# Optimization experiments

Measured on AMD Instinct MI355X. Metric: run time of the kernel, lower is better.

The kernel has to match this reference:

```python
import jax, jax.numpy as jnp
import numpy as np
import math

N = 50000      # nodes
E = 800000     # edges
D = 128        # hidden_dim
H = 8          # num_heads
HD = D // H    # head_dim
EPS = 1e-5


def setup_inputs() -> dict:
    key = jax.random.key(0)
    ks = jax.random.split(key, 24)
    s = 0.02
    inp = {
        "x": jax.random.normal(ks[0], (N, D), jnp.float32),
        "edge_index": jax.random.randint(ks[1], (2, E), 0, N, jnp.int64),
        "edge_attr": jax.random.normal(ks[2], (E, D), jnp.float32),
        # attention projections (stored [in, out]; torch Linear is x @ W.T + b)
        "Wq": jax.random.normal(ks[3], (D, D), jnp.float32) * s,
        "bq": jnp.zeros((D,), jnp.float32),
        "Wk": jax.random.normal(ks[4], (D, D), jnp.float32) * s,
        "bk": jnp.zeros((D,), jnp.float32),
        "Wv": jax.random.normal(ks[5], (D, D), jnp.float32) * s,
        "bv": jnp.zeros((D,), jnp.float32),
        "Wo": jax.random.normal(ks[6], (D, D), jnp.float32) * s,
        "bo": jnp.zeros((D,), jnp.float32),
        # edge-feature -> per-head score bias
        "We": jax.random.normal(ks[7], (D, H), jnp.float32) * s,
        "be": jnp.zeros((H,), jnp.float32),
        # FFN
        "W1": jax.random.normal(ks[8], (D, 4 * D), jnp.float32) * s,
        "bf1": jnp.zeros((4 * D,), jnp.float32),
        "W2": jax.random.normal(ks[9], (4 * D, D), jnp.float32) * s,
        "bf2": jnp.zeros((D,), jnp.float32),
        # layer norms
        "g1": jnp.ones((D,), jnp.float32),
        "beta1": jnp.zeros((D,), jnp.float32),
        "g2": jnp.ones((D,), jnp.float32),
        "beta2": jnp.zeros((D,), jnp.float32),
    }
    return inp


def _layer_norm(x, g, b):
    m = jnp.mean(x, axis=-1, keepdims=True)
    v = jnp.mean(jnp.square(x - m), axis=-1, keepdims=True)
    return (x - m) * jax.lax.rsqrt(v + EPS) * g + b


def reference(x, edge_index, edge_attr, Wq, bq, Wk, bk, Wv, bv, Wo, bo,
              We, be, W1, bf1, W2, bf2, g1, beta1, g2, beta2):
    row, col = edge_index[0], edge_index[1]

    # --- pre-norm attention block ---
    xn = _layer_norm(x, g1, beta1)
    Q = (xn @ Wq + bq).reshape(N, H, HD)
    K = (xn @ Wk + bk).reshape(N, H, HD)
    V = (xn @ Wv + bv).reshape(N, H, HD)

    # per-edge dot-product scores [E, H]
    scores = jnp.einsum('ehd,ehd->eh', Q[row], K[col]) / math.sqrt(HD)
    scores = scores + edge_attr @ We + be

    # segment softmax over edges grouped by destination node `row`
    smax = jax.ops.segment_max(scores, row, num_segments=N)  # [N, H]
    smax = jax.lax.stop_gradient(smax)
    ex = jnp.exp(scores - smax[row])
    denom = jax.ops.segment_sum(ex, row, num_segments=N)     # [N, H]
    alpha = ex / denom[row]                                  # [E, H]

    # weighted scatter-add aggregation [N, H, HD]
    agg = jax.ops.segment_sum(V[col] * alpha[..., None], row, num_segments=N)
    attn_out = agg.reshape(N, D) @ Wo + bo
    x = x + attn_out

    # --- pre-norm FFN block ---
    xn2 = _layer_norm(x, g2, beta2)
    h = jax.nn.gelu(xn2 @ W1 + bf1, approximate=False)
    x = x + (h @ W2 + bf2)
    return x
```

## Files before the change

kernel.cpp:

```cpp
#include <hip/hip_runtime.h>
#include <hip/hip_bf16.h>
#include <math.h>

#define NNODES 50000
#define NEDGES 800000
#define DIM 128
#define NH 8

#define NEG_SENTINEL -3.0e38f

typedef __attribute__((ext_vector_type(8))) short bf16x8_t;
typedef __attribute__((ext_vector_type(4))) float f32x4_t;

__device__ __forceinline__ float gelu_exact(float v) {
    return 0.5f * v * (1.0f + erff(v * 0.70710678118654752f));
}
__device__ __forceinline__ ushort bfbits(float f) {
    uint u = __float_as_uint(f);
    u += 0x7fffu + ((u >> 16) & 1u);
    return (ushort)(u >> 16);
}
__device__ __forceinline__ uint pack2(float a, float b) {
    return (uint)bfbits(a) | ((uint)bfbits(b) << 16);
}
__device__ __forceinline__ float lo16(uint u) { return __uint_as_float(u << 16); }
__device__ __forceinline__ float hi16(uint u) { return __uint_as_float(u & 0xffff0000u); }
__device__ __forceinline__ float b2f(ushort u) { return __uint_as_float(((uint)u) << 16); }

__global__ void zero_counts(int* __restrict__ counts) {
    int i = blockIdx.x * 256 + threadIdx.x;
    if (i < NNODES) counts[i] = 0;
}

__global__ void setup_kernel(const int* __restrict__ ei, int* __restrict__ counts,
                             int* __restrict__ rank,
                             const float* __restrict__ Wq, const float* __restrict__ Wk,
                             const float* __restrict__ Wv, const float* __restrict__ Wo,
                             const float* __restrict__ W1, const float* __restrict__ W2,
                             const float* __restrict__ We,
                             const float* __restrict__ bq, const float* __restrict__ bk,
                             const float* __restrict__ bv,
                             ushort* __restrict__ wt4, ushort* __restrict__ w1t,
                             ushort* __restrict__ w2t, ushort* __restrict__ wet,
                             float* __restrict__ b384) {
    int b = blockIdx.x;
    if (b < NEDGES / 256) {
        int e = b * 256 + threadIdx.x;
        rank[e] = atomicAdd(&counts[ei[e]], 1);
        return;
    }
    int i = (b - NEDGES / 256) * 256 + threadIdx.x;
    if (i < 65536) {
        int w = i >> 14, j = i & 16383;
        int c = j >> 7, k = j & 127;
        const float* src = (w == 0) ? Wq : (w == 1) ? Wk : (w == 2) ? Wv : Wo;
        wt4[i] = bfbits(src[k * 128 + c]);
    } else if (i < 131072) {
        int j = i - 65536;
        int c = j >> 7, k = j & 127;
        w1t[j] = bfbits(W1[k * 512 + c]);
    } else if (i < 196608) {
        int j = i - 131072;
        int c = j >> 9, k = j & 511;
        w2t[j] = bfbits(W2[k * 128 + c]);
    } else if (i < 198656) {
        int j = i - 196608;
        int h = j >> 7, k = j & 127;
        wet[j] = (h < 8) ? bfbits(We[k * 8 + h]) : (ushort)0;
    } else if (i < 198656 + 384) {
        int j = i - 198656;
        b384[j] = (j < 128) ? bq[j] : (j < 256) ? bk[j - 128] : bv[j - 256];
    }
}

__global__ __launch_bounds__(256)
void ln_qkv_kernel(const float* __restrict__ x, const float* __restrict__ g1,
                   const float* __restrict__ b1, const ushort* __restrict__ wt4,
                   const float* __restrict__ b384, ushort* __restrict__ Qb,
                   uint* __restrict__ KVp, int M) {
    __shared__ ushort An[64 * 128];
    __shared__ ushort Ws[64 * 128];
    int tid = threadIdx.x, lane = tid & 63, wave = tid >> 6;
    int row0b = blockIdx.x * 64;
    int sr = lane >> 4;
    int sl = lane & 15;
    char* WsB = reinterpret_cast<char*>(Ws);
    float4 ga = reinterpret_cast<const float4*>(g1)[sl * 2];
    float4 gb = reinterpret_cast<const float4*>(g1)[sl * 2 + 1];
    float4 ba = reinterpret_cast<const float4*>(b1)[sl * 2];
    float4 bbv = reinterpret_cast<const float4*>(b1)[sl * 2 + 1];
    #pragma unroll
    for (int g = 0; g < 4; ++g) {
        int rl = wave * 16 + g * 4 + sr;
        int srow = min(row0b + rl, M - 1);
        const float4* xp = reinterpret_cast<const float4*>(x + (size_t)srow * 128 + sl * 8);
        float4 a = xp[0], b = xp[1];
        float s  = ((a.x + a.y) + (a.z + a.w)) + ((b.x + b.y) + (b.z + b.w));
        float sq = ((a.x*a.x + a.y*a.y) + (a.z*a.z + a.w*a.w)) +
                   ((b.x*b.x + b.y*b.y) + (b.z*b.z + b.w*b.w));
        #pragma unroll
        for (int mm = 1; mm < 16; mm <<= 1) {
            s  += __shfl_xor(s, mm, 64);
            sq += __shfl_xor(sq, mm, 64);
        }
        float mean = s * (1.0f / DIM);
        float var  = sq * (1.0f / DIM) - mean * mean;
        float rs = rsqrtf(var + 1e-5f);
        uint4 pk;
        pk.x = pack2((a.x - mean) * rs * ga.x + ba.x, (a.y - mean) * rs * ga.y + ba.y);
        pk.y = pack2((a.z - mean) * rs * ga.z + ba.z, (a.w - mean) * rs * ga.w + ba.w);
        pk.z = pack2((b.x - mean) * rs * gb.x + bbv.x, (b.y - mean) * rs * gb.y + bbv.y);
        pk.w = pack2((b.z - mean) * rs * gb.z + bbv.z, (b.w - mean) * rs * gb.w + bbv.w);
        int byte = rl * 256 + ((sl * 16) ^ ((rl & 7) << 4));
        *reinterpret_cast<uint4*>(reinterpret_cast<char*>(An) + byte) = pk;
    }
    __builtin_amdgcn_wave_barrier();
    int er = lane & 15, kg = lane >> 4;
    int lrow = wave * 16 + er;
    int rsw = (er & 7) << 4;
    bf16x8_t afN[4];
    #pragma unroll
    for (int ks = 0; ks < 4; ++ks)
        afN[ks] = *reinterpret_cast<const bf16x8_t*>(
            reinterpret_cast<char*>(An) + lrow * 256 + ((ks * 64 + kg * 16) ^ rsw));
    f32x4_t acc[24];
    #pragma unroll
    for (int f = 0; f < 24; ++f) acc[f] = (f32x4_t){0.f, 0.f, 0.f, 0.f};
    #pragma unroll
    for (int st = 0; st < 6; ++st) {
        __syncthreads();
        #pragma unroll
        for (int it = 0; it < 4; ++it) {
            int idx = it * 256 + tid;
            int col = idx >> 4, ch = idx & 15;
            uint4 d = *reinterpret_cast<const uint4*>(wt4 + (size_t)(st * 64 + col) * 128 + ch * 8);
            *reinterpret_cast<uint4*>(WsB + col * 256 + ((ch * 16) ^ ((col & 7) << 4))) = d;
        }
        __syncthreads();
        #pragma unroll
        for (int ks = 0; ks < 4; ++ks) {
            #pragma unroll
            for (int fl = 0; fl < 4; ++fl) {
                int fc = fl * 16 + er;
                bf16x8_t bfr = *reinterpret_cast<const bf16x8_t*>(
                    WsB + fc * 256 + ((ks * 64 + kg * 16) ^ ((fc & 7) << 4)));
                acc[st * 4 + fl] = __builtin_amdgcn_mfma_f32_16x16x32_bf16(afN[ks], bfr, acc[st * 4 + fl], 0, 0, 0);
            }
        }
    }
    #pragma unroll
    for (int f = 0; f < 24; ++f) {
        int col = (f >> 2) * 64 + (f & 3) * 16 + er;
        float bc = b384[col];
        #pragma unroll
        for (int r = 0; r < 4; ++r) {
            int row = row0b + wave * 16 + kg * 4 + r;
            if (row < M) {
                float v = acc[f][r] + bc;
                if (col < 128) {
                    Qb[(size_t)row * 128 + col] = bfbits(v);
                } else if (col < 256) {
                    reinterpret_cast<ushort*>(KVp + (size_t)row * 128 + (col - 128))[0] = bfbits(v);
                } else {
                    reinterpret_cast<ushort*>(KVp + (size_t)row * 128 + (col - 256))[1] = bfbits(v);
                }
            }
        }
    }
}

__global__ __launch_bounds__(256)
void wo_ffn_kernel(const ushort* __restrict__ A, const ushort* __restrict__ woT,
                   const float* __restrict__ bo, const float* __restrict__ xres,
                   const float* __restrict__ g2, const float* __restrict__ b2,
                   const ushort* __restrict__ w1t, const float* __restrict__ bf1,
                   const ushort* __restrict__ w2t, const float* __restrict__ bf2,
                   float* __restrict__ out, int M) {
    __shared__ ushort An[64 * 128];
    __shared__ ushort Hb[64 * 128];
    __shared__ ushort Ws[64 * 128];
    int tid = threadIdx.x, lane = tid & 63, wave = tid >> 6;
    int row0 = blockIdx.x * 64 + wave * 16;
    int er = lane & 15, kg = lane >> 4;
    int arow = min(row0 + er, M - 1);
    char* WsB = reinterpret_cast<char*>(Ws);

    f32x4_t acc[8];
    #pragma unroll
    for (int f = 0; f < 8; ++f) acc[f] = (f32x4_t){0.f, 0.f, 0.f, 0.f};
    bf16x8_t afA[4];
    #pragma unroll
    for (int ks = 0; ks < 4; ++ks)
        afA[ks] = *reinterpret_cast<const bf16x8_t*>(A + (size_t)arow * 128 + ks * 32 + kg * 8);
    #pragma unroll
    for (int hh = 0; hh < 2; ++hh) {
        __syncthreads();
        #pragma unroll
        for (int it = 0; it < 4; ++it) {
            int idx = it * 256 + tid;
            int col = idx >> 4, ch = idx & 15;
            uint4 d = *reinterpret_cast<const uint4*>(woT + (size_t)(hh * 64 + col) * 128 + ch * 8);
            *reinterpret_cast<uint4*>(WsB + col * 256 + ((ch * 16) ^ ((col & 7) << 4))) = d;
        }
        __syncthreads();
        #pragma unroll
        for (int ks = 0; ks < 4; ++ks) {
            #pragma unroll
            for (int fl = 0; fl < 4; ++fl) {
                int fc = fl * 16 + er;
                bf16x8_t bfr = *reinterpret_cast<const bf16x8_t*>(
                    WsB + fc * 256 + ((ks * 64 + kg * 16) ^ ((fc & 7) << 4)));
                acc[hh * 4 + fl] = __builtin_amdgcn_mfma_f32_16x16x32_bf16(afA[ks], bfr, acc[hh * 4 + fl], 0, 0, 0);
            }
        }
    }
    float g2l[8], b2l[8];
    #pragma unroll
    for (int f = 0; f < 8; ++f) {
        int col = (f >> 2) * 64 + (f & 3) * 16 + er;
        float bc = bo[col];
        g2l[f] = g2[col]; b2l[f] = b2[col];
        #pragma unroll
        for (int r = 0; r < 4; ++r) {
            int row = min(row0 + kg * 4 + r, M - 1);
            acc[f][r] += bc + xres[(size_t)row * 128 + col];
        }
    }
    #pragma unroll
    for (int r = 0; r < 4; ++r) {
        float s = 0.f, sq = 0.f;
        #pragma unroll
        for (int f = 0; f < 8; ++f) { s += acc[f][r]; sq += acc[f][r] * acc[f][r]; }
        #pragma unroll
        for (int m = 1; m < 16; m <<= 1) {
            s  += __shfl_xor(s, m, 64);
            sq += __shfl_xor(sq, m, 64);
        }
        float mean = s * (1.0f / DIM);
        float var  = sq * (1.0f / DIM) - mean * mean;
        float rs = rsqrtf(var + 1e-5f);
        int rl = wave * 16 + kg * 4 + r;
        #pragma unroll
        for (int f = 0; f < 8; ++f) {
            int col = (f >> 2) * 64 + (f & 3) * 16 + er;
            float xv = (acc[f][r] - mean) * rs * g2l[f] + b2l[f];
            int byte = rl * 256 + ((col * 2) ^ ((rl & 7) << 4));
            *reinterpret_cast<ushort*>(reinterpret_cast<char*>(An) + byte) = bfbits(xv);
        }
    }
    __builtin_amdgcn_wave_barrier();

    int lrow = wave * 16 + er;
    int rsw = (lrow & 7) << 4;
    f32x4_t acc2[8];
    #pragma unroll
    for (int f = 0; f < 8; ++f) acc2[f] = (f32x4_t){0.f, 0.f, 0.f, 0.f};

    bf16x8_t afN[4];
    #pragma unroll
    for (int ks = 0; ks < 4; ++ks)
        afN[ks] = *reinterpret_cast<const bf16x8_t*>(
            reinterpret_cast<char*>(An) + lrow * 256 + ((ks * 64 + kg * 16) ^ rsw));

    for (int q = 0; q < 4; ++q) {
        f32x4_t acch[8];
        #pragma unroll
        for (int f = 0; f < 8; ++f) acch[f] = (f32x4_t){0.f, 0.f, 0.f, 0.f};
        #pragma unroll
        for (int hh = 0; hh < 2; ++hh) {
            __syncthreads();
            #pragma unroll
            for (int it = 0; it < 4; ++it) {
                int idx = it * 256 + tid;
                int col = idx >> 4, ch = idx & 15;
                uint4 d = *reinterpret_cast<const uint4*>(
                    w1t + (size_t)(q * 128 + hh * 64 + col) * 128 + ch * 8);
                *reinterpret_cast<uint4*>(WsB + col * 256 + ((ch * 16) ^ ((col & 7) << 4))) = d;
            }
            __syncthreads();
            #pragma unroll
            for (int ks = 0; ks < 4; ++ks) {
                #pragma unroll
                for (int fl = 0; fl < 4; ++fl) {
                    int fc = fl * 16 + er;
                    bf16x8_t bfr = *reinterpret_cast<const bf16x8_t*>(
                        WsB + fc * 256 + ((ks * 64 + kg * 16) ^ ((fc & 7) << 4)));
                    acch[hh * 4 + fl] = __builtin_amdgcn_mfma_f32_16x16x32_bf16(afN[ks], bfr, acch[hh * 4 + fl], 0, 0, 0);
                }
            }
        }
        #pragma unroll
        for (int f = 0; f < 8; ++f) {
            int colq = (f >> 2) * 64 + (f & 3) * 16 + er;
            float bc = bf1[q * 128 + colq];
            #pragma unroll
            for (int r = 0; r < 4; ++r) {
                int rl2 = wave * 16 + kg * 4 + r;
                float hv = gelu_exact(acch[f][r] + bc);
                int byte = rl2 * 256 + ((colq * 2) ^ ((rl2 & 7) << 4));
                *reinterpret_cast<ushort*>(reinterpret_cast<char*>(Hb) + byte) = bfbits(hv);
            }
        }
        __builtin_amdgcn_wave_barrier();
        bf16x8_t afH[4];
        #pragma unroll
        for (int ks = 0; ks < 4; ++ks)
            afH[ks] = *reinterpret_cast<const bf16x8_t*>(
                reinterpret_cast<char*>(Hb) + lrow * 256 + ((ks * 64 + kg * 16) ^ rsw));
        #pragma unroll
        for (int hh = 0; hh < 2; ++hh) {
            __syncthreads();
            #pragma unroll
            for (int it = 0; it < 4; ++it) {
                int idx = it * 256 + tid;
                int col = idx >> 4, ch = idx & 15;
                uint4 d = *reinterpret_cast<const uint4*>(
                    w2t + (size_t)(hh * 64 + col) * 512 + q * 128 + ch * 8);
                *reinterpret_cast<uint4*>(WsB + col * 256 + ((ch * 16) ^ ((col & 7) << 4))) = d;
            }
            __syncthreads();
            #pragma unroll
            for (int ks2 = 0; ks2 < 4; ++ks2) {
                #pragma unroll
                for (int fl = 0; fl < 4; ++fl) {
                    int fc = fl * 16 + er;
                    bf16x8_t bfr = *reinterpret_cast<const bf16x8_t*>(
                        WsB + fc * 256 + ((ks2 * 64 + kg * 16) ^ ((fc & 7) << 4)));
                    acc2[hh * 4 + fl] = __builtin_amdgcn_mfma_f32_16x16x32_bf16(afH[ks2], bfr, acc2[hh * 4 + fl], 0, 0, 0);
                }
            }
        }
    }
    #pragma unroll
    for (int f = 0; f < 8; ++f) {
        int col = (f >> 2) * 64 + (f & 3) * 16 + er;
        float bc = bf2[col];
        #pragma unroll
        for (int r = 0; r < 4; ++r) {
            int row = row0 + kg * 4 + r;
            if (row < M) out[(size_t)row * 128 + col] = acc2[f][r] + bc + acc[f][r];
        }
    }
}

#define SCAN_BLOCKS ((NNODES + 255) / 256)
__global__ void scan_ph1(const int* __restrict__ counts, int* __restrict__ rowstart,
                         int* __restrict__ blocksum) {
    __shared__ int sh[256];
    int t = threadIdx.x, i = blockIdx.x * 256 + t;
    int c = (i < NNODES) ? counts[i] : 0;
    sh[t] = c; __syncthreads();
    int v = c;
    #pragma unroll
    for (int off = 1; off < 256; off <<= 1) {
        int u = (t >= off) ? sh[t - off] : 0;
        __syncthreads();
        v += u; sh[t] = v;
        __syncthreads();
    }
    if (i < NNODES) rowstart[i] = v - c;
    if (t == 255) blocksum[blockIdx.x] = v;
}
__global__ void scan_ph2(const int* __restrict__ blocksum, int* __restrict__ blockoff) {
    __shared__ int sh[256];
    int t = threadIdx.x;
    int c = (t < SCAN_BLOCKS) ? blocksum[t] : 0;
    sh[t] = c; __syncthreads();
    int v = c;
    #pragma unroll
    for (int off = 1; off < 256; off <<= 1) {
        int u = (t >= off) ? sh[t - off] : 0;
        __syncthreads();
        v += u; sh[t] = v;
        __syncthreads();
    }
    if (t < SCAN_BLOCKS) blockoff[t] = v - c;
}

#define EB_TILES (NEDGES / 64)
__global__ __launch_bounds__(256)
void edge_bias_scatter(const float* __restrict__ EA, const ushort* __restrict__ wet,
                       const float* __restrict__ be, const int* __restrict__ ei,
                       const int* __restrict__ rowstart, const int* __restrict__ blockoff,
                       const int* __restrict__ rank,
                       ushort* __restrict__ ebs_sorted, int* __restrict__ col_sorted) {
    __shared__ ushort lds[64 * 128];
    int tid = threadIdx.x, lane = tid & 63, wave = tid >> 6;
    int er = lane & 15, kg = lane >> 4;
    int lrow = wave * 16 + er;
    float beh = be[er & 7];
    int stride = gridDim.x;
    int tile = blockIdx.x;
    float4 r[8];
    if (tile < EB_TILES) {
        const float4* src = reinterpret_cast<const float4*>(EA + (size_t)tile * 64 * 128);
        #pragma unroll
        for (int it = 0; it < 8; ++it) r[it] = src[it * 256 + tid];
    }
    for (; tile < EB_TILES; tile += stride) {
        #pragma unroll
        for (int it = 0; it < 8; ++it) {
            int idx = it * 256 + tid;
            int elem = idx * 4;
            int row = elem >> 7, col = elem & 127;
            uint2 pk;
            pk.x = pack2(r[it].x, r[it].y);
            pk.y = pack2(r[it].z, r[it].w);
            int byte = row * 256 + ((col * 2) ^ ((row & 7) << 4));
            *reinterpret_cast<uint2*>(reinterpret_cast<char*>(lds) + byte) = pk;
        }
        __syncthreads();
        int ntile = tile + stride;
        if (ntile < EB_TILES) {
            const float4* src = reinterpret_cast<const float4*>(EA + (size_t)ntile * 64 * 128);
            #pragma unroll
            for (int it = 0; it < 8; ++it) r[it] = src[it * 256 + tid];
        }
        f32x4_t acc = (f32x4_t){0.f, 0.f, 0.f, 0.f};
        #pragma unroll
        for (int ks = 0; ks < 4; ++ks) {
            int cb = (ks * 64 + kg * 16) ^ ((er & 7) << 4);
            bf16x8_t af = *reinterpret_cast<const bf16x8_t*>(
                reinterpret_cast<char*>(lds) + lrow * 256 + cb);
            bf16x8_t bfr = *reinterpret_cast<const bf16x8_t*>(wet + er * 128 + ks * 32 + kg * 8);
            acc = __builtin_amdgcn_mfma_f32_16x16x32_bf16(af, bfr, acc, 0, 0, 0);
        }
        int e0 = tile * 64 + wave * 16;
        int pos = 0;
        if (lane < 16) {
            int e = e0 + lane;
            int row = ei[e], col = ei[NEDGES + e];
            pos = rowstart[row] + blockoff[row >> 8] + rank[e];
            col_sorted[pos] = col;
        }
        #pragma unroll
        for (int rr = 0; rr < 4; ++rr) {
            int pj = __shfl(pos, kg * 4 + rr, 64);
            if (er < 8) ebs_sorted[(size_t)pj * 8 + er] = bfbits(acc[rr] + beh);
        }
        __syncthreads();
    }
}

__global__ __launch_bounds__(256)
void attn_node_kernel(const int* __restrict__ rowstart, const int* __restrict__ blockoff,
                      const int* __restrict__ col_sorted,
                      const ushort* __restrict__ ebs_sorted, const ushort* __restrict__ Qb,
                      const uint* __restrict__ KVp, ushort* __restrict__ agg) {
    int wave = threadIdx.x >> 6;
    int lane = threadIdx.x & 63;
    int n = blockIdx.x * 4 + wave;
    if (n >= NNODES) return;
    int s0 = rowstart[n] + blockoff[n >> 8];
    int s1 = (n + 1 == NNODES) ? NEDGES : rowstart[n + 1] + blockoff[(n + 1) >> 8];
    int h = lane >> 3;

    uint qu = *reinterpret_cast<const uint*>(Qb + (size_t)n * 128 + lane * 2);
    float q0 = lo16(qu), q1 = hi16(qu);

    float m = NEG_SENTINEL, ssum = 0.f, a0 = 0.f, a1 = 0.f;
    int p = s0;
    for (; p + 8 <= s1; p += 8) {
        int cc[8]; uint2 kv[8]; float ebv[8], dd[8];
        #pragma unroll
        for (int i = 0; i < 8; ++i) cc[i] = col_sorted[p + i];
        #pragma unroll
        for (int i = 0; i < 8; ++i)
            kv[i] = *reinterpret_cast<const uint2*>(KVp + (size_t)cc[i] * 128 + lane * 2);
        #pragma unroll
        for (int i = 0; i < 8; ++i) ebv[i] = b2f(ebs_sorted[(size_t)(p + i) * 8 + h]);
        #pragma unroll
        for (int i = 0; i < 8; ++i) {
            float d = q0 * lo16(kv[i].x) + q1 * lo16(kv[i].y);
            d += __shfl_xor(d, 1, 64);
            d += __shfl_xor(d, 2, 64);
            d += __shfl_xor(d, 4, 64);
            dd[i] = d * 0.25f + ebv[i];
        }
        float mx = m;
        #pragma unroll
        for (int i = 0; i < 8; ++i) mx = fmaxf(mx, dd[i]);
        float sc = __expf(m - mx);
        float pv[8];
        #pragma unroll
        for (int i = 0; i < 8; ++i) pv[i] = __expf(dd[i] - mx);
        float psum = ((pv[0] + pv[1]) + (pv[2] + pv[3])) + ((pv[4] + pv[5]) + (pv[6] + pv[7]));
        float v0 = 0.f, v1 = 0.f;
        #pragma unroll
        for (int i = 0; i < 8; ++i) {
            v0 += pv[i] * hi16(kv[i].x);
            v1 += pv[i] * hi16(kv[i].y);
        }
        ssum = ssum * sc + psum;
        a0 = a0 * sc + v0;
        a1 = a1 * sc + v1;
        m = mx;
    }
    for (; p + 4 <= s1; p += 4) {
        int cc[4]; uint2 kv[4]; float ebv[4], dd[4];
        #pragma unroll
        for (int i = 0; i < 4; ++i) cc[i] = col_sorted[p + i];
        #pragma unroll
        for (int i = 0; i < 4; ++i)
            kv[i] = *reinterpret_cast<const uint2*>(KVp + (size_t)cc[i] * 128 + lane * 2);
        #pragma unroll
        for (int i = 0; i < 4; ++i) ebv[i] = b2f(ebs_sorted[(size_t)(p + i) * 8 + h]);
        #pragma unroll
        for (int i = 0; i < 4; ++i) {
            float d = q0 * lo16(kv[i].x) + q1 * lo16(kv[i].y);
            d += __shfl_xor(d, 1, 64);
            d += __shfl_xor(d, 2, 64);
            d += __shfl_xor(d, 4, 64);
            dd[i] = d * 0.25f + ebv[i];
        }
        float mx = fmaxf(fmaxf(fmaxf(dd[0], dd[1]), fmaxf(dd[2], dd[3])), m);
        float sc = __expf(m - mx);
        float p0 = __expf(dd[0] - mx), p1 = __expf(dd[1] - mx);
        float p2 = __expf(dd[2] - mx), p3 = __expf(dd[3] - mx);
        ssum = ssum * sc + ((p0 + p1) + (p2 + p3));
        a0 = a0 * sc + p0 * hi16(kv[0].x) + p1 * hi16(kv[1].x) + p2 * hi16(kv[2].x) + p3 * hi16(kv[3].x);
        a1 = a1 * sc + p0 * hi16(kv[0].y) + p1 * hi16(kv[1].y) + p2 * hi16(kv[2].y) + p3 * hi16(kv[3].y);
        m = mx;
    }
    for (; p < s1; ++p) {
        int c = col_sorted[p];
        uint2 kv = *reinterpret_cast<const uint2*>(KVp + (size_t)c * 128 + lane * 2);
        float eb = b2f(ebs_sorted[(size_t)p * 8 + h]);
        float d = q0 * lo16(kv.x) + q1 * lo16(kv.y);
        d += __shfl_xor(d, 1, 64);
        d += __shfl_xor(d, 2, 64);
        d += __shfl_xor(d, 4, 64);
        float s = d * 0.25f + eb;
        float mn = fmaxf(m, s);
        float sc = __expf(m - mn);
        float pv = __expf(s - mn);
        ssum = ssum * sc + pv;
        a0 = a0 * sc + pv * hi16(kv.x);
        a1 = a1 * sc + pv * hi16(kv.y);
        m = mn;
    }
    float inv = (ssum > 0.f) ? 1.0f / ssum : 0.f;
    reinterpret_cast<uint*>(agg + (size_t)n * 128)[lane] = pack2(a0 * inv, a1 * inv);
}

extern "C" void kernel_launch(void* const* d_in, const int* in_sizes, int n_in,
                              void* d_out, int out_size, void* d_ws, size_t ws_size,
                              hipStream_t stream) {
    const float* x   = (const float*)d_in[0];
    const int*   ei  = (const int*)d_in[1];
    const float* ea  = (const float*)d_in[2];
    const float* Wq  = (const float*)d_in[3];  const float* bq  = (const float*)d_in[4];
    const float* Wk  = (const float*)d_in[5];  const float* bk  = (const float*)d_in[6];
    const float* Wv  = (const float*)d_in[7];  const float* bv  = (const float*)d_in[8];
    const float* Wo  = (const float*)d_in[9];  const float* bo  = (const float*)d_in[10];
    const float* We  = (const float*)d_in[11]; const float* be  = (const float*)d_in[12];
    const float* W1  = (const float*)d_in[13]; const float* bf1 = (const float*)d_in[14];
    const float* W2  = (const float*)d_in[15]; const float* bf2 = (const float*)d_in[16];
    const float* g1  = (const float*)d_in[17]; const float* b1  = (const float*)d_in[18];
    const float* g2  = (const float*)d_in[19]; const float* b2  = (const float*)d_in[20];

    char* base = (char*)d_ws;
    ushort* agg       = (ushort*)(base);
    ushort* Qb        = (ushort*)(base + 12800000);
    uint*   KVp       = (uint*)(base + 25600000);
    ushort* ebs_sorted= (ushort*)(base + 51200000);
    int*    col_sorted= (int*)(base + 64000000);
    int*    rank      = (int*)(base + 67200000);
    int*    counts    = (int*)(base + 70400000);
    int*    rowstart  = (int*)(base + 70600000);
    ushort* wt4       = (ushort*)(base + 70800016);
    ushort* w1t       = (ushort*)(base + 70931088);
    ushort* w2t       = (ushort*)(base + 71062160);
    ushort* wet       = (ushort*)(base + 71193232);
    float*  b384      = (float*)(base + 71197328);
    int*    blocksum  = (int*)(base + 71198864);
    int*    blockoff  = (int*)(base + 71199648);

    zero_counts<<<(NNODES + 255) / 256, 256, 0, stream>>>(counts);

    setup_kernel<<<NEDGES / 256 + 778, 256, 0, stream>>>(ei, counts, rank, Wq, Wk, Wv, Wo,
                                                         W1, W2, We, bq, bk, bv,
                                                         wt4, w1t, w2t, wet, b384);

    dim3 g128((NNODES + 63) / 64, 1);
    ln_qkv_kernel<<<g128, 256, 0, stream>>>(x, g1, b1, wt4, b384, Qb, KVp, NNODES);

    scan_ph1<<<SCAN_BLOCKS, 256, 0, stream>>>(counts, rowstart, blocksum);
    scan_ph2<<<1, 256, 0, stream>>>(blocksum, blockoff);

    edge_bias_scatter<<<2048, 256, 0, stream>>>(ea, wet, be, ei, rowstart, blockoff, rank,
                                                ebs_sorted, col_sorted);
    attn_node_kernel<<<(NNODES + 3) / 4, 256, 0, stream>>>(rowstart, blockoff, col_sorted,
                                                           ebs_sorted, Qb, KVp, agg);

    wo_ffn_kernel<<<g128, 256, 0, stream>>>(agg, wt4 + 49152, bo, x, g2, b2,
                                            w1t, bf1, w2t, bf2, (float*)d_out, NNODES);
}
```

Measured before the change: 330.2 us.

## Register-prefetch weight tiles in GEMM kernels and fuse two-phase scan

```diff
diff --git a/kernel.cpp b/kernel.cpp
--- a/kernel.cpp
+++ b/kernel.cpp
@@ -27,9 +27,34 @@
 __device__ __forceinline__ float hi16(uint u) { return __uint_as_float(u & 0xffff0000u); }
 __device__ __forceinline__ float b2f(ushort u) { return __uint_as_float(((uint)u) << 16); }
 
+__device__ __forceinline__ void stage_load(const ushort* base, int strideRow, uint4* wreg, int tid) {
+    #pragma unroll
+    for (int it = 0; it < 4; ++it) {
+        int idx = it * 256 + tid;
+        int col = idx >> 4, ch = idx & 15;
+        wreg[it] = *reinterpret_cast<const uint4*>(base + (size_t)col * strideRow + ch * 8);
+    }
+}
+__device__ __forceinline__ void stage_write(char* WsB, const uint4* wreg, int tid) {
+    #pragma unroll
+    for (int it = 0; it < 4; ++it) {
+        int idx = it * 256 + tid;
+        int col = idx >> 4, ch = idx & 15;
+        *reinterpret_cast<uint4*>(WsB + col * 256 + ((ch * 16) ^ ((col & 7) << 4))) = wreg[it];
+    }
+}
+__device__ __forceinline__ const ushort* wf_stage_ptr(int s, const ushort* woT,
+                                                      const ushort* w1t, const ushort* w2t,
+                                                      int* stride) {
+    if (s < 2) { *stride = 128; return woT + (size_t)s * 64 * 128; }
+    int t = s - 2; int q = t >> 2, k = t & 3;
+    if (k < 2) { *stride = 128; return w1t + (size_t)(q * 128 + k * 64) * 128; }
+    *stride = 512; return w2t + (size_t)(k - 2) * 64 * 512 + q * 128;
+}
+
 __global__ void zero_counts(int* __restrict__ counts) {
     int i = blockIdx.x * 256 + threadIdx.x;
-    if (i < NNODES) counts[i] = 0;
+    if (i < NNODES + 1) counts[i] = 0;
 }
 
 __global__ void setup_kernel(const int* __restrict__ ei, int* __restrict__ counts,
@@ -85,6 +110,8 @@
     int sr = lane >> 4;
     int sl = lane & 15;
     char* WsB = reinterpret_cast<char*>(Ws);
+    uint4 wreg[4];
+    stage_load(wt4, 128, wreg, tid);
     float4 ga = reinterpret_cast<const float4*>(g1)[sl * 2];
     float4 gb = reinterpret_cast<const float4*>(g1)[sl * 2 + 1];
     float4 ba = reinterpret_cast<const float4*>(b1)[sl * 2];
@@ -129,13 +156,8 @@
     #pragma unroll
     for (int st = 0; st < 6; ++st) {
         __syncthreads();
-        #pragma unroll
-        for (int it = 0; it < 4; ++it) {
-            int idx = it * 256 + tid;
-            int col = idx >> 4, ch = idx & 15;
-            uint4 d = *reinterpret_cast<const uint4*>(wt4 + (size_t)(st * 64 + col) * 128 + ch * 8);
-            *reinterpret_cast<uint4*>(WsB + col * 256 + ((ch * 16) ^ ((col & 7) << 4))) = d;
-        }
+        stage_write(WsB, wreg, tid);
+        if (st < 5) stage_load(wt4 + (size_t)(st + 1) * 64 * 128, 128, wreg, tid);
         __syncthreads();
         #pragma unroll
         for (int ks = 0; ks < 4; ++ks) {
@@ -185,6 +207,12 @@
     int arow = min(row0 + er, M - 1);
     char* WsB = reinterpret_cast<char*>(Ws);
 
+    uint4 wreg[4];
+    {
+        int strd; const ushort* p = wf_stage_ptr(0, woT, w1t, w2t, &strd);
+        stage_load(p, strd, wreg, tid);
+    }
+
     f32x4_t acc[8];
     #pragma unroll
     for (int f = 0; f < 8; ++f) acc[f] = (f32x4_t){0.f, 0.f, 0.f, 0.f};
@@ -192,15 +220,15 @@
     #pragma unroll
     for (int ks = 0; ks < 4; ++ks)
         afA[ks] = *reinterpret_cast<const bf16x8_t*>(A + (size_t)arow * 128 + ks * 32 + kg * 8);
+
     #pragma unroll
     for (int hh = 0; hh < 2; ++hh) {
         __syncthreads();
-        #pragma unroll
-        for (int it = 0; it < 4; ++it) {
-            int idx = it * 256 + tid;
-            int col = idx >> 4, ch = idx & 15;
-            uint4 d = *reinterpret_cast<const uint4*>(woT + (size_t)(hh * 64 + col) * 128 + ch * 8);
-            *reinterpret_cast<uint4*>(WsB + col * 256 + ((ch * 16) ^ ((col & 7) << 4))) = d;
+        stage_write(WsB, wreg, tid);
+        {
+            int ns = hh + 1, strd;
+            const ushort* p = wf_stage_ptr(ns, woT, w1t, w2t, &strd);
+            stage_load(p, strd, wreg, tid);
         }
         __syncthreads();
         #pragma unroll
@@ -269,13 +297,11 @@
         #pragma unroll
         for (int hh = 0; hh < 2; ++hh) {
             __syncthreads();
-            #pragma unroll
-            for (int it = 0; it < 4; ++it) {
-                int idx = it * 256 + tid;
-                int col = idx >> 4, ch = idx & 15;
-                uint4 d = *reinterpret_cast<const uint4*>(
-                    w1t + (size_t)(q * 128 + hh * 64 + col) * 128 + ch * 8);
-                *reinterpret_cast<uint4*>(WsB + col * 256 + ((ch * 16) ^ ((col & 7) << 4))) = d;
+            stage_write(WsB, wreg, tid);
+            {
+                int ns = 2 + q * 4 + hh + 1, strd;
+                const ushort* p = wf_stage_ptr(ns, woT, w1t, w2t, &strd);
+                stage_load(p, strd, wreg, tid);
             }
             __syncthreads();
             #pragma unroll
@@ -310,13 +336,13 @@
         #pragma unroll
         for (int hh = 0; hh < 2; ++hh) {
             __syncthreads();
-            #pragma unroll
-            for (int it = 0; it < 4; ++it) {
-                int idx = it * 256 + tid;
-                int col = idx >> 4, ch = idx & 15;
-                uint4 d = *reinterpret_cast<const uint4*>(
-                    w2t + (size_t)(hh * 64 + col) * 512 + q * 128 + ch * 8);
-                *reinterpret_cast<uint4*>(WsB + col * 256 + ((ch * 16) ^ ((col & 7) << 4))) = d;
+            stage_write(WsB, wreg, tid);
+            {
+                int ns = 2 + q * 4 + 2 + hh + 1, strd;
+                if (ns < 18) {
+                    const ushort* p = wf_stage_ptr(ns, woT, w1t, w2t, &strd);
+                    stage_load(p, strd, wreg, tid);
+                }
             }
             __syncthreads();
             #pragma unroll
@@ -344,9 +370,11 @@
 }
 
 #define SCAN_BLOCKS ((NNODES + 255) / 256)
-__global__ void scan_ph1(const int* __restrict__ counts, int* __restrict__ rowstart,
-                         int* __restrict__ blocksum) {
+__global__ void scan_kernel(const int* __restrict__ counts, int* __restrict__ rowstart,
+                            int* __restrict__ blocksum, int* __restrict__ blockoff,
+                            int* __restrict__ done_ctr) {
     __shared__ int sh[256];
+    __shared__ int isLast;
     int t = threadIdx.x, i = blockIdx.x * 256 + t;
     int c = (i < NNODES) ? counts[i] : 0;
     sh[t] = c; __syncthreads();
@@ -360,21 +388,23 @@
     }
     if (i < NNODES) rowstart[i] = v - c;
     if (t == 255) blocksum[blockIdx.x] = v;
-}
-__global__ void scan_ph2(const int* __restrict__ blocksum, int* __restrict__ blockoff) {
-    __shared__ int sh[256];
-    int t = threadIdx.x;
-    int c = (t < SCAN_BLOCKS) ? blocksum[t] : 0;
-    sh[t] = c; __syncthreads();
-    int v = c;
+    __threadfence();
+    if (t == 0) isLast = (atomicAdd(done_ctr, 1) == gridDim.x - 1);
+    __syncthreads();
+    if (!isLast) return;
+    volatile const int* bs = blocksum;
+    int c2 = (t < SCAN_BLOCKS) ? bs[t] : 0;
+    __syncthreads();
+    sh[t] = c2; __syncthreads();
+    int v2 = c2;
     #pragma unroll
     for (int off = 1; off < 256; off <<= 1) {
         int u = (t >= off) ? sh[t - off] : 0;
         __syncthreads();
-        v += u; sh[t] = v;
-        __syncthreads();
-    }
-    if (t < SCAN_BLOCKS) blockoff[t] = v - c;
+        v2 += u; sh[t] = v2;
+        __syncthreads();
+    }
+    if (t < SCAN_BLOCKS) blockoff[t] = v2 - c2;
 }
 
 #define EB_TILES (NEDGES / 64)
@@ -567,7 +597,8 @@
     int*    col_sorted= (int*)(base + 64000000);
     int*    rank      = (int*)(base + 67200000);
     int*    counts    = (int*)(base + 70400000);
-    int*    rowstart  = (int*)(base + 70600000);
+    int*    done_ctr  = counts + NNODES;
+    int*    rowstart  = (int*)(base + 70600004);
     ushort* wt4       = (ushort*)(base + 70800016);
     ushort* w1t       = (ushort*)(base + 70931088);
     ushort* w2t       = (ushort*)(base + 71062160);
@@ -576,7 +607,7 @@
     int*    blocksum  = (int*)(base + 71198864);
     int*    blockoff  = (int*)(base + 71199648);
 
-    zero_counts<<<(NNODES + 255) / 256, 256, 0, stream>>>(counts);
+    zero_counts<<<(NNODES + 256) / 256, 256, 0, stream>>>(counts);
 
     setup_kernel<<<NEDGES / 256 + 778, 256, 0, stream>>>(ei, counts, rank, Wq, Wk, Wv, Wo,
                                                          W1, W2, We, bq, bk, bv,
@@ -585,8 +616,7 @@
     dim3 g128((NNODES + 63) / 64, 1);
     ln_qkv_kernel<<<g128, 256, 0, stream>>>(x, g1, b1, wt4, b384, Qb, KVp, NNODES);
 
-    scan_ph1<<<SCAN_BLOCKS, 256, 0, stream>>>(counts, rowstart, blocksum);
-    scan_ph2<<<1, 256, 0, stream>>>(blocksum, blockoff);
+    scan_kernel<<<SCAN_BLOCKS, 256, 0, stream>>>(counts, rowstart, blocksum, blockoff, done_ctr);
 
     edge_bias_scatter<<<2048, 256, 0, stream>>>(ea, wet, be, ei, rowstart, blockoff, rank,
                                                 ebs_sorted, col_sorted);
```

Measured after the change: 406.0 us. +22.9%, slower.
